# Optimization experiments

Hardware: AMD Instinct MI355X
Metric: run time of the kernel (lower is better)

## Reference

```python
import jax, jax.numpy as jnp
import numpy as np

N_NODES = 100000
NEG_SLOPE = 0.2

def _glorot(key, shape):
    lim = float(np.sqrt(6.0 / (shape[0] + shape[-1])))
    return jax.random.uniform(key, shape, jnp.float32, -lim, lim)

def setup_inputs() -> dict:
    key = jax.random.key(0)
    ks = jax.random.split(key, 12)
    x = jax.random.normal(ks[0], (N_NODES, 128), jnp.float32)
    edge_index = jax.random.randint(ks[1], (2, 3200000), 0, N_NODES).astype(jnp.int64)
    # layer 1: in=128, heads=2, out=8
    W1 = _glorot(ks[2], (128, 16)); a_src1 = _glorot(ks[3], (2, 8)); a_dst1 = _glorot(ks[4], (2, 8)); b1 = jnp.zeros((16,), jnp.float32)
    # layer 2: in=16, heads=2, out=4
    W2 = _glorot(ks[5], (16, 8)); a_src2 = _glorot(ks[6], (2, 4)); a_dst2 = _glorot(ks[7], (2, 4)); b2 = jnp.zeros((8,), jnp.float32)
    # layer 3: in=8, heads=1, out=4
    W3 = _glorot(ks[8], (8, 4)); a_src3 = _glorot(ks[9], (1, 4)); a_dst3 = _glorot(ks[10], (1, 4)); b3 = jnp.zeros((4,), jnp.float32)
    Wc = _glorot(ks[11], (4, 2)); bc = jnp.zeros((2,), jnp.float32)
    return {"x": x, "edge_index": edge_index,
            "W1": W1, "a_src1": a_src1, "a_dst1": a_dst1, "b1": b1,
            "W2": W2, "a_src2": a_src2, "a_dst2": a_dst2, "b2": b2,
            "W3": W3, "a_src3": a_src3, "a_dst3": a_dst3, "b3": b3,
            "Wc": Wc, "bc": bc}

def gat_layer(x, src, dst, W, a_src, a_dst, b, H, C):
    # PyG GATConv: linear -> per-node attention terms -> per-edge leaky_relu -> segment softmax over dst -> scatter-sum
    N = x.shape[0]
    h = (x @ W).reshape(N, H, C)                         # [N,H,C]
    alpha_s = jnp.sum(h * a_src, axis=-1)                # [N,H]
    alpha_d = jnp.sum(h * a_dst, axis=-1)                # [N,H]
    e = jax.nn.leaky_relu(alpha_s[src] + alpha_d[dst], NEG_SLOPE)  # [E,H]
    m = jax.ops.segment_max(e, dst, num_segments=N)      # [N,H]
    ex = jnp.exp(e - m[dst])
    denom = jax.ops.segment_sum(ex, dst, num_segments=N)
    alpha = ex / (denom[dst] + 1e-16)                    # [E,H]
    out = jax.ops.segment_sum(h[src] * alpha[:, :, None], dst, num_segments=N)  # [N,H,C]
    return out.reshape(N, H * C) + b

def reference(x, edge_index, W1, a_src1, a_dst1, b1, W2, a_src2, a_dst2, b2, W3, a_src3, a_dst3, b3, Wc, bc):
    N = x.shape[0]
    loop = jnp.arange(N, dtype=edge_index.dtype)
    src = jnp.concatenate([edge_index[0], loop])  # add_self_loops=True (PyG default)
    dst = jnp.concatenate([edge_index[1], loop])
    h = jax.nn.relu(gat_layer(x, src, dst, W1, a_src1, a_dst1, b1, 2, 8))
    h = jax.nn.relu(gat_layer(h, src, dst, W2, a_src2, a_dst2, b2, 2, 4))
    # dropout p=0.5 is identity in eval mode
    h = gat_layer(h, src, dst, W3, a_src3, a_dst3, b3, 1, 4)
    return h @ Wc + bc
```

## Files before the change

kernel.cpp:

```cpp
#include <hip/hip_runtime.h>

#define TB 256
#define NGRP 8
#define NB_P 512
#define TBP 256
#define NBKT 256
#define SORT_T 1024
#define STG_CAP 14336
#define STG2_CAP 6656

typedef int      i4v __attribute__((ext_vector_type(4)));
typedef float    f4v __attribute__((ext_vector_type(4)));
typedef _Float16 h4v __attribute__((ext_vector_type(4)));
typedef _Float16 h8v __attribute__((ext_vector_type(8)));

struct __align__(16) Rec2 { _Float16 h[8]; float as[2]; float pad[2]; };
struct __align__(16) Rec3 { _Float16 h[4]; float as; float pad; };

static __device__ __forceinline__ float leaky(float x) {
  return x > 0.f ? x : 0.2f * x;
}


__global__ void __launch_bounds__(TB)
k_scatter_node1(const int* __restrict__ srcA, const int* __restrict__ dstA,
                int* __restrict__ cnt, int* __restrict__ loffG,
                int* __restrict__ epkPriv, int E4, int E, unsigned M, int R,
                int CH4, int CHP,
                const float* __restrict__ xin, const float* __restrict__ W1,
                const float* __restrict__ a_src, const float* __restrict__ a_dst,
                _Float16* __restrict__ hout, float* __restrict__ as_,
                float* __restrict__ ad_, int N) {
  __shared__ __align__(16) char smem[33552];
  const int t = threadIdx.x;
  if (blockIdx.x < NB_P) {
    const int kblk = blockIdx.x;
    int* lc   = (int*)smem;
    int* loff = (int*)(smem + 4096);
    int* lcur = (int*)(smem + 5136);
    int* stg  = (int*)(smem + 6160);
    for (int i = t; i < 4 * NBKT; i += TBP) lc[i] = 0;
    __syncthreads();
    int* lcw = lc + (t >> 6) * NBKT;
    const int bstart = kblk * CH4;
    const int bend = min(E4, bstart + CH4);
    const i4v* d4 = reinterpret_cast<const i4v*>(dstA);
    const i4v* s4 = reinterpret_cast<const i4v*>(srcA);
    for (int i = bstart + t; i < bend; i += TBP) {
      i4v d = d4[i];
#pragma unroll
      for (int k = 0; k < 4; ++k) atomicAdd(&lcw[__umulhi((unsigned)d[k], M)], 1);
    }
    if (kblk == NB_P - 1) {
      for (int i = E4 * 4 + t; i < E; i += TBP)
        atomicAdd(&lcw[__umulhi((unsigned)dstA[i], M)], 1);
    }
    __syncthreads();
    int c = 0;
    if (t < NBKT) {
      c = lc[t] + lc[NBKT + t] + lc[2 * NBKT + t] + lc[3 * NBKT + t];
      loff[t] = c;
    }
    __syncthreads();
    for (int o = 1; o < NBKT; o <<= 1) {
      int u = (t < NBKT && t >= o) ? loff[t - o] : 0;
      __syncthreads();
      if (t < NBKT) loff[t] += u;
      __syncthreads();
    }
    if (t < NBKT) {
      int excl = loff[t] - c;
      cnt[t * NB_P + kblk] = c;
      loffG[kblk * NBKT + t] = excl;
      lcur[t] = excl;
      loff[t] = excl;
      if (t == NBKT - 1) loff[NBKT] = excl + c;
    }
    __syncthreads();
    for (int i = bstart + t; i < bend; i += TBP) {
      i4v d = d4[i];
      i4v sv = __builtin_nontemporal_load(&s4[i]);
#pragma unroll
      for (int k = 0; k < 4; ++k) {
        int dd = d[k];
        int b = __umulhi((unsigned)dd, M);
        int pos = atomicAdd(&lcur[b], 1);
        stg[pos] = ((dd - b * R) << 17) | sv[k];
      }
    }
    if (kblk == NB_P - 1) {
      for (int i = E4 * 4 + t; i < E; i += TBP) {
        int dd = dstA[i];
        int b = __umulhi((unsigned)dd, M);
        int pos = atomicAdd(&lcur[b], 1);
        stg[pos] = ((dd - b * R) << 17) | srcA[i];
      }
    }
    __syncthreads();
    const int total = loff[NBKT];
    int* dst = epkPriv + (size_t)kblk * CHP;
    for (int i = t; i < total; i += TBP) dst[i] = stg[i];
  } else {
    constexpr int IN = 128, OUT = 16, SPLIT = 4, NPB = TB / SPLIT, PIN4 = IN / SPLIT / 4;
    float* Ws = (float*)smem;
    float* As = (float*)(smem + 8192);
    float* Ad = (float*)(smem + 8256);
    const int bid = blockIdx.x - NB_P;
    for (int i = t; i < IN * OUT; i += TB) Ws[i] = W1[i];
    if (t < OUT) {
      As[t] = a_src[t];
      Ad[t] = a_dst[t];
    }
    __syncthreads();
    const int j = t & (SPLIT - 1);
    const int n = bid * NPB + t / SPLIT;
    if (n >= N) return;
    float acc[OUT];
#pragma unroll
    for (int q = 0; q < OUT; ++q) acc[q] = 0.f;
    const f4v* x4 = reinterpret_cast<const f4v*>(xin + (size_t)n * IN + j * (IN / SPLIT));
#pragma unroll
    for (int k4 = 0; k4 < PIN4; ++k4) {
      f4v xv = __builtin_nontemporal_load(&x4[k4]);
      const int kb = j * (IN / SPLIT) + 4 * k4;
#pragma unroll
      for (int q = 0; q < OUT; ++q) {
        acc[q] += xv[0] * Ws[(kb + 0) * OUT + q];
        acc[q] += xv[1] * Ws[(kb + 1) * OUT + q];
        acc[q] += xv[2] * Ws[(kb + 2) * OUT + q];
        acc[q] += xv[3] * Ws[(kb + 3) * OUT + q];
      }
    }
#pragma unroll
    for (int o = 1; o < SPLIT; o <<= 1) {
#pragma unroll
      for (int q = 0; q < OUT; ++q) acc[q] += __shfl_xor(acc[q], o);
    }
    if (j < OUT / 4) {
      h4v v;
      v[0] = (_Float16)acc[4 * j + 0];
      v[1] = (_Float16)acc[4 * j + 1];
      v[2] = (_Float16)acc[4 * j + 2];
      v[3] = (_Float16)acc[4 * j + 3];
      reinterpret_cast<h4v*>(hout + (size_t)n * OUT)[j] = v;
    }
    if (j < 2) {
      float ss = 0.f, dd = 0.f;
#pragma unroll
      for (int c = 0; c < 8; ++c) {
        ss += acc[j * 8 + c] * As[j * 8 + c];
        dd += acc[j * 8 + c] * Ad[j * 8 + c];
      }
      as_[n * 2 + j] = ss;
      ad_[n * 2 + j] = dd;
    }
  }
}

__global__ void k_bscan1(const int* __restrict__ cnt, int* __restrict__ off,
                         int* __restrict__ colTotal) {
  __shared__ int sh[NB_P];
  const int t = threadIdx.x;
  const int b = blockIdx.x;
  int v = cnt[b * NB_P + t];
  sh[t] = v;
  __syncthreads();
  for (int o = 1; o < NB_P; o <<= 1) {
    int u = (t >= o) ? sh[t - o] : 0;
    __syncthreads();
    sh[t] += u;
    __syncthreads();
  }
  off[b * NB_P + t] = sh[t] - v;
  if (t == NB_P - 1) colTotal[b] = sh[t];
}

__global__ void k_bscan2(const int* __restrict__ colTotal, int* __restrict__ bucketBase) {
  __shared__ int sh[NBKT];
  const int t = threadIdx.x;
  int v = colTotal[t];
  sh[t] = v;
  __syncthreads();
  for (int o = 1; o < NBKT; o <<= 1) {
    int u = (t >= o) ? sh[t - o] : 0;
    __syncthreads();
    sh[t] += u;
    __syncthreads();
  }
  bucketBase[t] = sh[t] - v;
  if (t == NBKT - 1) bucketBase[NBKT] = sh[t];
}

__global__ void k_bsort(const int* __restrict__ epkPriv, const int* __restrict__ off,
                        const int* __restrict__ loffG, const int* __restrict__ bucketBase,
                        int* __restrict__ rowStart, int* __restrict__ colIdx,
                        int N, int R, int E, int CHP) {
  __shared__ int offRow[NB_P];
  __shared__ int loffCol[NB_P];
  __shared__ int sc[512];
  __shared__ int stg[STG_CAP];
  const int b = (blockIdx.x & (NGRP - 1)) * (NBKT / NGRP) + (blockIdx.x >> 3);
  const int lo = bucketBase[b], hi = bucketBase[b + 1];
  const int cntB = hi - lo;
  const int nodeLo = b * R;
  const int nN = min(R, N - nodeLo);
  const int t = threadIdx.x;
  if (t < NB_P) {
    offRow[t] = off[b * NB_P + t];
    loffCol[t] = loffG[t * NBKT + b];
  }
  if (t < 512) sc[t] = 0;
  __syncthreads();
  auto fetch = [&](int i) -> int {
    int loQ = 0, hiQ = NB_P;
#pragma unroll
    for (int it = 0; it < 9; ++it) {
      int mid = (loQ + hiQ) >> 1;
      if (offRow[mid] <= i) loQ = mid; else hiQ = mid;
    }
    return epkPriv[(size_t)loQ * CHP + loffCol[loQ] + (i - offRow[loQ])];
  };
  for (int i = t; i < cntB; i += SORT_T) {
    int pk = fetch(i);
    atomicAdd(&sc[pk >> 17], 1);
  }
  __syncthreads();
  int own = (t < 512) ? sc[t] : 0;
  for (int o = 1; o < 512; o <<= 1) {
    int u = (t < 512 && t >= o) ? sc[t - o] : 0;
    __syncthreads();
    if (t < 512) sc[t] += u;
    __syncthreads();
  }
  if (t < nN) rowStart[nodeLo + t] = lo + sc[t] - own;
  if (b == NBKT - 1 && t == 0) rowStart[N] = E;
  if (t < 512) sc[t] -= own;
  __syncthreads();
  for (int i = t; i < cntB; i += SORT_T) {
    int pk = fetch(i);
    int pos = atomicAdd(&sc[pk >> 17], 1);
    stg[pos] = pk & 0x1FFFF;
  }
  __syncthreads();
  for (int i = t; i < cntB; i += SORT_T) colIdx[lo + i] = stg[i];
}


__global__ void k_edge12(const int* __restrict__ rowStart, const int* __restrict__ colIdx,
                         const _Float16* __restrict__ h1, const float* __restrict__ as_,
                         const float* __restrict__ ad_, const float* __restrict__ b1,
                         const float* __restrict__ W2, const float* __restrict__ as2w,
                         const float* __restrict__ ad2w, Rec2* __restrict__ r2,
                         float* __restrict__ ad2, int N, int R8) {
  constexpr int L = 2, S = 4, LS = 8, NPB = TB / LS;
  __shared__ float Ws2[128], A2s[8], A2d[8], B1s[16];
  if (threadIdx.x < 128) Ws2[threadIdx.x] = W2[threadIdx.x];
  if (threadIdx.x < 8) {
    A2s[threadIdx.x] = as2w[threadIdx.x];
    A2d[threadIdx.x] = ad2w[threadIdx.x];
  }
  if (threadIdx.x < 16) B1s[threadIdx.x] = b1[threadIdx.x];
  __syncthreads();
  const int g = blockIdx.x & (NGRP - 1);
  const int lb = blockIdx.x / NGRP;
  const int lane = threadIdx.x % LS;
  const int sub = lane >> 1;
  const int j = lane & 1;
  const int n = g * R8 + lb * NPB + threadIdx.x / LS;
  const int nEnd = min((g + 1) * R8, N);
  if (n >= nEnd) return;
  const float adv = ad_[n * 2 + j];
  const int start = rowStart[n];
  const int end = rowStart[n + 1];
  float s = 0.f, acc[8];
#pragma unroll
  for (int q = 0; q < 8; ++q) acc[q] = 0.f;
  if (sub == 0) {
    float p = __expf(leaky(as_[n * 2 + j] + adv));
    h8v a0 = reinterpret_cast<const h8v*>(h1 + (size_t)n * 16)[j];
    s = p;
#pragma unroll
    for (int q = 0; q < 8; ++q) acc[q] = p * (float)a0[q];
  }
  const int base = start & ~3;
  const int nch = (end - base + 3) >> 2;
  i4v cv;
  if (sub < nch) cv = *reinterpret_cast<const i4v*>(colIdx + base + 4 * sub);
  for (int t = sub; t < nch; t += S) {
    i4v nxt = cv;
    if (t + S < nch) nxt = *reinterpret_cast<const i4v*>(colIdx + base + 4 * (t + S));
    const int i0 = base + 4 * t;
#pragma unroll
    for (int k = 0; k < 4; ++k) {
      const bool ok = (i0 + k >= start) && (i0 + k < end);
      const int src = ok ? cv[k] : n;
      h8v hv = reinterpret_cast<const h8v*>(h1 + (size_t)src * 16)[j];
      float e = as_[src * 2 + j];
      float p = ok ? __expf(leaky(e + adv)) : 0.f;
      s += p;
#pragma unroll
      for (int q = 0; q < 8; ++q) acc[q] += p * (float)hv[q];
    }
    cv = nxt;
  }
#pragma unroll
  for (int off = L; off < LS; off <<= 1) {
    s += __shfl_xor(s, off);
#pragma unroll
    for (int q = 0; q < 8; ++q) acc[q] += __shfl_xor(acc[q], off);
  }
  if (sub == 0) {
    float inv = 1.f / (s + 1e-16f);
    float o1v[8];
#pragma unroll
    for (int q = 0; q < 8; ++q) o1v[q] = fmaxf(acc[q] * inv + B1s[j * 8 + q], 0.f);
    float h2p[8];
#pragma unroll
    for (int q = 0; q < 8; ++q) {
      float tacc = 0.f;
#pragma unroll
      for (int c = 0; c < 8; ++c) tacc += o1v[c] * Ws2[(j * 8 + c) * 8 + q];
      h2p[q] = tacc;
    }
    float h2f[8];
#pragma unroll
    for (int q = 0; q < 8; ++q) h2f[q] = h2p[q] + __shfl_xor(h2p[q], 1);
    h4v v;
#pragma unroll
    for (int q = 0; q < 4; ++q) v[q] = (_Float16)h2f[j * 4 + q];
    reinterpret_cast<h4v*>(r2[n].h)[j] = v;
    float ss = 0.f, dd = 0.f;
#pragma unroll
    for (int c = 0; c < 4; ++c) {
      ss += h2f[j * 4 + c] * A2s[j * 4 + c];
      dd += h2f[j * 4 + c] * A2d[j * 4 + c];
    }
    r2[n].as[j] = ss;
    ad2[n * 2 + j] = dd;
  }
}


__global__ void k_edge23(const int* __restrict__ rowStart, const int* __restrict__ colIdx,
                         const Rec2* __restrict__ r2, const float* __restrict__ ad_,
                         const float* __restrict__ b2, const float* __restrict__ W3,
                         const float* __restrict__ as3w, const float* __restrict__ ad3w,
                         Rec3* __restrict__ r3, float* __restrict__ ad3, int N, int R8) {
  constexpr int L = 2, S = 4, LS = 8, NPB = TB / LS;
  __shared__ float Ws3[32], A3s[4], A3d[4], B2s[8];
  if (threadIdx.x < 32) Ws3[threadIdx.x] = W3[threadIdx.x];
  if (threadIdx.x < 4) {
    A3s[threadIdx.x] = as3w[threadIdx.x];
    A3d[threadIdx.x] = ad3w[threadIdx.x];
  }
  if (threadIdx.x < 8) B2s[threadIdx.x] = b2[threadIdx.x];
  __syncthreads();
  const int g = blockIdx.x & (NGRP - 1);
  const int lb = blockIdx.x / NGRP;
  const int lane = threadIdx.x % LS;
  const int sub = lane >> 1;
  const int j = lane & 1;
  const int n = g * R8 + lb * NPB + threadIdx.x / LS;
  const int nEnd = min((g + 1) * R8, N);
  if (n >= nEnd) return;
  const float adv = ad_[n * 2 + j];
  const int start = rowStart[n];
  const int end = rowStart[n + 1];
  float s = 0.f, acc[4];
#pragma unroll
  for (int q = 0; q < 4; ++q) acc[q] = 0.f;
  if (sub == 0) {
    float p = __expf(leaky(r2[n].as[j] + adv));
    h4v a0 = reinterpret_cast<const h4v*>(r2[n].h)[j];
    s = p;
#pragma unroll
    for (int q = 0; q < 4; ++q) acc[q] = p * (float)a0[q];
  }
  const int base = start & ~3;
  const int nch = (end - base + 3) >> 2;
  i4v cv;
  if (sub < nch) cv = *reinterpret_cast<const i4v*>(colIdx + base + 4 * sub);
  for (int t = sub; t < nch; t += S) {
    i4v nxt = cv;
    if (t + S < nch) nxt = *reinterpret_cast<const i4v*>(colIdx + base + 4 * (t + S));
    const int i0 = base + 4 * t;
#pragma unroll
    for (int k = 0; k < 4; ++k) {
      const bool ok = (i0 + k >= start) && (i0 + k < end);
      const int src = ok ? cv[k] : n;
      h4v hv = reinterpret_cast<const h4v*>(r2[src].h)[j];
      float e = r2[src].as[j];
      float p = ok ? __expf(leaky(e + adv)) : 0.f;
      s += p;
#pragma unroll
      for (int q = 0; q < 4; ++q) acc[q] += p * (float)hv[q];
    }
    cv = nxt;
  }
#pragma unroll
  for (int off = L; off < LS; off <<= 1) {
    s += __shfl_xor(s, off);
#pragma unroll
    for (int q = 0; q < 4; ++q) acc[q] += __shfl_xor(acc[q], off);
  }
  if (sub == 0) {
    float inv = 1.f / (s + 1e-16f);
    float o2v[4];
#pragma unroll
    for (int q = 0; q < 4; ++q) o2v[q] = fmaxf(acc[q] * inv + B2s[j * 4 + q], 0.f);
    float h3p[4];
#pragma unroll
    for (int q = 0; q < 4; ++q) {
      float tacc = 0.f;
#pragma unroll
      for (int c = 0; c < 4; ++c) tacc += o2v[c] * Ws3[(j * 4 + c) * 4 + q];
      h3p[q] = tacc;
    }
    float h3f[4];
#pragma unroll
    for (int q = 0; q < 4; ++q) h3f[q] = h3p[q] + __shfl_xor(h3p[q], 1);
    if (j == 0) {
      Rec3 rec;
#pragma unroll
      for (int q = 0; q < 4; ++q) rec.h[q] = (_Float16)h3f[q];
      float ss = 0.f, dd = 0.f;
#pragma unroll
      for (int c = 0; c < 4; ++c) {
        ss += h3f[c] * A3s[c];
        dd += h3f[c] * A3d[c];
      }
      rec.as = ss;
      rec.pad = 0.f;
      r3[n] = rec;
      ad3[n] = dd;
    }
  }
}


__global__ void k_edge3(const int* __restrict__ rowStart, const int* __restrict__ colIdx,
                        const Rec3* __restrict__ r3, const float* __restrict__ ad_,
                        const float* __restrict__ b3, const float* __restrict__ Wc,
                        const float* __restrict__ bc, float* __restrict__ out,
                        int N, int R8) {
  constexpr int S = 8;
  constexpr int NPB = TB / S;
  const int g = blockIdx.x & (NGRP - 1);
  const int lb = blockIdx.x / NGRP;
  const int sub = threadIdx.x % S;
  const int n = g * R8 + lb * NPB + threadIdx.x / S;
  const int nEnd = min((g + 1) * R8, N);
  if (n >= nEnd) return;
  const float adv = ad_[n];
  const int start = rowStart[n];
  const int end = rowStart[n + 1];
  float s = 0.f, acc0 = 0.f, acc1 = 0.f, acc2 = 0.f, acc3 = 0.f;
  if (sub == 0) {
    Rec3 rec = r3[n];
    float p = __expf(leaky(rec.as + adv));
    s = p;
    acc0 = p * (float)rec.h[0];
    acc1 = p * (float)rec.h[1];
    acc2 = p * (float)rec.h[2];
    acc3 = p * (float)rec.h[3];
  }
  const int base = start & ~3;
  const int nch = (end - base + 3) >> 2;
  i4v cv;
  if (sub < nch) cv = *reinterpret_cast<const i4v*>(colIdx + base + 4 * sub);
  for (int t = sub; t < nch; t += S) {
    i4v nxt = cv;
    if (t + S < nch) nxt = *reinterpret_cast<const i4v*>(colIdx + base + 4 * (t + S));
    const int i0 = base + 4 * t;
#pragma unroll
    for (int k = 0; k < 4; ++k) {
      const bool ok = (i0 + k >= start) && (i0 + k < end);
      const int src = ok ? cv[k] : n;
      Rec3 rec = r3[src];
      float p = ok ? __expf(leaky(rec.as + adv)) : 0.f;
      s += p;
      acc0 += p * (float)rec.h[0];
      acc1 += p * (float)rec.h[1];
      acc2 += p * (float)rec.h[2];
      acc3 += p * (float)rec.h[3];
    }
    cv = nxt;
  }
#pragma unroll
  for (int off = 1; off < S; off <<= 1) {
    s += __shfl_xor(s, off);
    acc0 += __shfl_xor(acc0, off);
    acc1 += __shfl_xor(acc1, off);
    acc2 += __shfl_xor(acc2, off);
    acc3 += __shfl_xor(acc3, off);
  }
  if (sub == 0) {
    float inv = 1.f / (s + 1e-16f);
    float o0 = acc0 * inv + b3[0];
    float o1 = acc1 * inv + b3[1];
    float o2 = acc2 * inv + b3[2];
    float o3 = acc3 * inv + b3[3];
    float2 r;
    r.x = o0 * Wc[0] + o1 * Wc[2] + o2 * Wc[4] + o3 * Wc[6] + bc[0];
    r.y = o0 * Wc[1] + o1 * Wc[3] + o2 * Wc[5] + o3 * Wc[7] + bc[1];
    reinterpret_cast<float2*>(out)[n] = r;
  }
}


extern "C" void kernel_launch(void* const* d_in, const int* in_sizes, int n_in,
                              void* d_out, int out_size, void* d_ws, size_t ws_size,
                              hipStream_t stream) {
  const float* x    = (const float*)d_in[0];
  const int*   ei   = (const int*)d_in[1];
  const float* W1   = (const float*)d_in[2];
  const float* as1w = (const float*)d_in[3];
  const float* ad1w = (const float*)d_in[4];
  const float* b1   = (const float*)d_in[5];
  const float* W2   = (const float*)d_in[6];
  const float* as2w = (const float*)d_in[7];
  const float* ad2w = (const float*)d_in[8];
  const float* b2   = (const float*)d_in[9];
  const float* W3   = (const float*)d_in[10];
  const float* as3w = (const float*)d_in[11];
  const float* ad3w = (const float*)d_in[12];
  const float* b3   = (const float*)d_in[13];
  const float* Wc   = (const float*)d_in[14];
  const float* bc   = (const float*)d_in[15];
  float* out = (float*)d_out;

  const int N = in_sizes[0] / 128;
  const int E = in_sizes[1] / 2;
  const int* srcA = ei;
  const int* dstA = ei + E;

  char* p = (char*)d_ws;
  auto alloc = [&](size_t bytes) -> void* {
    void* r = (void*)p;
    p += (bytes + 255) & ~(size_t)255;
    return r;
  };
  const int E4  = E >> 2;
  const int CH4 = (E4 + NB_P - 1) / NB_P;
  const int CHP = CH4 * 4 + 8;

  int* cnt        = (int*)alloc((size_t)NBKT * NB_P * 4);
  int* off        = (int*)alloc((size_t)NBKT * NB_P * 4);
  int* loffG      = (int*)alloc((size_t)NB_P * NBKT * 4);
  int* colTotal   = (int*)alloc(NBKT * 4);
  int* bucketBase = (int*)alloc((NBKT + 1) * 4);
  int* rowStart   = (int*)alloc((size_t)(N + 1) * 4);
  int* epkPriv    = (int*)alloc((size_t)NB_P * CHP * 4);
  int* colIdx     = (int*)alloc((size_t)E * 4 + 256);
  _Float16* h1 = (_Float16*)alloc((size_t)N * 16 * 2);
  float* as1 = (float*)alloc((size_t)N * 2 * 4);
  float* ad1 = (float*)alloc((size_t)N * 2 * 4);
  Rec2* r2   = (Rec2*)alloc((size_t)N * sizeof(Rec2));
  float* ad2 = (float*)alloc((size_t)N * 2 * 4);
  Rec3* r3   = (Rec3*)alloc((size_t)N * sizeof(Rec3));
  float* ad3 = (float*)alloc((size_t)N * 4);

  const int R   = (N + NBKT - 1) / NBKT;
  const unsigned M = (unsigned)(((1ULL << 32) + R - 1) / R);
  const int R8  = R * (NBKT / NGRP);

  const int nb1 = (N + (TB / 4) - 1) / (TB / 4);
  const int ge8 = NGRP * ((R8 + (TB / 8) - 1) / (TB / 8));

  k_scatter_node1<<<NB_P + nb1, TB, 0, stream>>>(srcA, dstA, cnt, loffG, epkPriv,
                                                 E4, E, M, R, CH4, CHP,
                                                 x, W1, as1w, ad1w, h1, as1, ad1, N);
  k_bscan1<<<NBKT, NB_P, 0, stream>>>(cnt, off, colTotal);
  k_bscan2<<<1, NBKT, 0, stream>>>(colTotal, bucketBase);
  k_bsort<<<NBKT, SORT_T, 0, stream>>>(epkPriv, off, loffG, bucketBase, rowStart,
                                       colIdx, N, R, E, CHP);

  k_edge12<<<ge8, TB, 0, stream>>>(rowStart, colIdx, h1, as1, ad1, b1, W2, as2w, ad2w,
                                   r2, ad2, N, R8);
  k_edge23<<<ge8, TB, 0, stream>>>(rowStart, colIdx, r2, ad2, b2, W3, as3w, ad3w,
                                   r3, ad3, N, R8);
  k_edge3<<<ge8, TB, 0, stream>>>(rowStart, colIdx, r3, ad3, b3, Wc, bc, out, N, R8);
}
```

Before: 168.8 us.

## Double scatter blocks, cache edge loads in registers, recompute layer-1 source attention

Doubles the number of partition blocks in the bucket scatter and shrinks the per-block staging so more blocks fit per CU. The first pass now keeps up to four loaded dst/src vectors in registers so the second pass does not reload them from global memory. Layer-1 source attention is no longer stored per node; the edge kernel recomputes it from the fp16 features it already gathers, removing one random gather per edge. The bucket sort gains a direct-to-global fallback when a bucket overflows the shared staging buffer, and the scan kernel k_bscan1 is now launched with 1024 threads.

```diff
diff --git a/kernel.cpp b/kernel.cpp
--- a/kernel.cpp
+++ b/kernel.cpp
@@ -2,12 +2,13 @@
 
 #define TB 256
 #define NGRP 8
-#define NB_P 512
+#define NB_P 1024
 #define TBP 256
 #define NBKT 256
 #define SORT_T 1024
-#define STG_CAP 14336
-#define STG2_CAP 6656
+#define STG_CAP 13312
+#define STG2_CAP 3200
+#define RCAP 4
 
 typedef int      i4v __attribute__((ext_vector_type(4)));
 typedef float    f4v __attribute__((ext_vector_type(4)));
@@ -29,9 +30,8 @@
                 int CH4, int CHP,
                 const float* __restrict__ xin, const float* __restrict__ W1,
                 const float* __restrict__ a_src, const float* __restrict__ a_dst,
-                _Float16* __restrict__ hout, float* __restrict__ as_,
-                float* __restrict__ ad_, int N) {
-  __shared__ __align__(16) char smem[33552];
+                _Float16* __restrict__ hout, float* __restrict__ ad_, int N) {
+  __shared__ __align__(16) char smem[18960];
   const int t = threadIdx.x;
   if (blockIdx.x < NB_P) {
     const int kblk = blockIdx.x;
@@ -46,8 +46,12 @@
     const int bend = min(E4, bstart + CH4);
     const i4v* d4 = reinterpret_cast<const i4v*>(dstA);
     const i4v* s4 = reinterpret_cast<const i4v*>(srcA);
-    for (int i = bstart + t; i < bend; i += TBP) {
-      i4v d = d4[i];
+    i4v dr[RCAP], sr[RCAP];
+    int it1 = 0;
+    for (int i = bstart + t; i < bend; i += TBP, ++it1) {
+      i4v d = __builtin_nontemporal_load(&d4[i]);
+      i4v sv = __builtin_nontemporal_load(&s4[i]);
+      if (it1 < RCAP) { dr[it1] = d; sr[it1] = sv; }
 #pragma unroll
       for (int k = 0; k < 4; ++k) atomicAdd(&lcw[__umulhi((unsigned)d[k], M)], 1);
     }
@@ -77,9 +81,10 @@
       if (t == NBKT - 1) loff[NBKT] = excl + c;
     }
     __syncthreads();
-    for (int i = bstart + t; i < bend; i += TBP) {
-      i4v d = d4[i];
-      i4v sv = __builtin_nontemporal_load(&s4[i]);
+    int it2 = 0;
+    for (int i = bstart + t; i < bend; i += TBP, ++it2) {
+      i4v d = (it2 < RCAP) ? dr[it2] : d4[i];
+      i4v sv = (it2 < RCAP) ? sr[it2] : s4[i];
 #pragma unroll
       for (int k = 0; k < 4; ++k) {
         int dd = d[k];
@@ -103,14 +108,10 @@
   } else {
     constexpr int IN = 128, OUT = 16, SPLIT = 4, NPB = TB / SPLIT, PIN4 = IN / SPLIT / 4;
     float* Ws = (float*)smem;
-    float* As = (float*)(smem + 8192);
-    float* Ad = (float*)(smem + 8256);
+    float* Ad = (float*)(smem + 8192);
     const int bid = blockIdx.x - NB_P;
     for (int i = t; i < IN * OUT; i += TB) Ws[i] = W1[i];
-    if (t < OUT) {
-      As[t] = a_src[t];
-      Ad[t] = a_dst[t];
-    }
+    if (t < OUT) Ad[t] = a_dst[t];
     __syncthreads();
     const int j = t & (SPLIT - 1);
     const int n = bid * NPB + t / SPLIT;
@@ -145,13 +146,9 @@
       reinterpret_cast<h4v*>(hout + (size_t)n * OUT)[j] = v;
     }
     if (j < 2) {
-      float ss = 0.f, dd = 0.f;
-#pragma unroll
-      for (int c = 0; c < 8; ++c) {
-        ss += acc[j * 8 + c] * As[j * 8 + c];
-        dd += acc[j * 8 + c] * Ad[j * 8 + c];
-      }
-      as_[n * 2 + j] = ss;
+      float dd = 0.f;
+#pragma unroll
+      for (int c = 0; c < 8; ++c) dd += acc[j * 8 + c] * Ad[j * 8 + c];
       ad_[n * 2 + j] = dd;
     }
   }
@@ -205,16 +202,16 @@
   const int nodeLo = b * R;
   const int nN = min(R, N - nodeLo);
   const int t = threadIdx.x;
-  if (t < NB_P) {
-    offRow[t] = off[b * NB_P + t];
-    loffCol[t] = loffG[t * NBKT + b];
+  for (int i = t; i < NB_P; i += SORT_T) {
+    offRow[i] = off[b * NB_P + i];
+    loffCol[i] = loffG[i * NBKT + b];
   }
   if (t < 512) sc[t] = 0;
   __syncthreads();
   auto fetch = [&](int i) -> int {
     int loQ = 0, hiQ = NB_P;
 #pragma unroll
-    for (int it = 0; it < 9; ++it) {
+    for (int it = 0; it < 10; ++it) {
       int mid = (loQ + hiQ) >> 1;
       if (offRow[mid] <= i) loQ = mid; else hiQ = mid;
     }
@@ -236,30 +233,41 @@
   if (b == NBKT - 1 && t == 0) rowStart[N] = E;
   if (t < 512) sc[t] -= own;
   __syncthreads();
-  for (int i = t; i < cntB; i += SORT_T) {
-    int pk = fetch(i);
-    int pos = atomicAdd(&sc[pk >> 17], 1);
-    stg[pos] = pk & 0x1FFFF;
-  }
-  __syncthreads();
-  for (int i = t; i < cntB; i += SORT_T) colIdx[lo + i] = stg[i];
+  if (cntB <= STG_CAP) {
+    for (int i = t; i < cntB; i += SORT_T) {
+      int pk = fetch(i);
+      int pos = atomicAdd(&sc[pk >> 17], 1);
+      stg[pos] = pk & 0x1FFFF;
+    }
+    __syncthreads();
+    for (int i = t; i < cntB; i += SORT_T) colIdx[lo + i] = stg[i];
+  } else {
+    for (int i = t; i < cntB; i += SORT_T) {
+      int pk = fetch(i);
+      int pos = lo + atomicAdd(&sc[pk >> 17], 1);
+      colIdx[pos] = pk & 0x1FFFF;
+    }
+  }
 }
 
 
 __global__ void k_edge12(const int* __restrict__ rowStart, const int* __restrict__ colIdx,
-                         const _Float16* __restrict__ h1, const float* __restrict__ as_,
+                         const _Float16* __restrict__ h1, const float* __restrict__ as1w,
                          const float* __restrict__ ad_, const float* __restrict__ b1,
                          const float* __restrict__ W2, const float* __restrict__ as2w,
                          const float* __restrict__ ad2w, Rec2* __restrict__ r2,
                          float* __restrict__ ad2, int N, int R8) {
   constexpr int L = 2, S = 4, LS = 8, NPB = TB / LS;
-  __shared__ float Ws2[128], A2s[8], A2d[8], B1s[16];
+  __shared__ float Ws2[128], A1s[16], A2s[8], A2d[8], B1s[16];
   if (threadIdx.x < 128) Ws2[threadIdx.x] = W2[threadIdx.x];
+  if (threadIdx.x < 16) {
+    A1s[threadIdx.x] = as1w[threadIdx.x];
+    B1s[threadIdx.x] = b1[threadIdx.x];
+  }
   if (threadIdx.x < 8) {
     A2s[threadIdx.x] = as2w[threadIdx.x];
     A2d[threadIdx.x] = ad2w[threadIdx.x];
   }
-  if (threadIdx.x < 16) B1s[threadIdx.x] = b1[threadIdx.x];
   __syncthreads();
   const int g = blockIdx.x & (NGRP - 1);
   const int lb = blockIdx.x / NGRP;
@@ -270,14 +278,20 @@
   const int nEnd = min((g + 1) * R8, N);
   if (n >= nEnd) return;
   const float adv = ad_[n * 2 + j];
+  float aw[8];
+#pragma unroll
+  for (int c = 0; c < 8; ++c) aw[c] = A1s[j * 8 + c];
   const int start = rowStart[n];
   const int end = rowStart[n + 1];
   float s = 0.f, acc[8];
 #pragma unroll
   for (int q = 0; q < 8; ++q) acc[q] = 0.f;
   if (sub == 0) {
-    float p = __expf(leaky(as_[n * 2 + j] + adv));
     h8v a0 = reinterpret_cast<const h8v*>(h1 + (size_t)n * 16)[j];
+    float e = 0.f;
+#pragma unroll
+    for (int c = 0; c < 8; ++c) e += (float)a0[c] * aw[c];
+    float p = __expf(leaky(e + adv));
     s = p;
 #pragma unroll
     for (int q = 0; q < 8; ++q) acc[q] = p * (float)a0[q];
@@ -295,7 +309,9 @@
       const bool ok = (i0 + k >= start) && (i0 + k < end);
       const int src = ok ? cv[k] : n;
       h8v hv = reinterpret_cast<const h8v*>(h1 + (size_t)src * 16)[j];
-      float e = as_[src * 2 + j];
+      float e = 0.f;
+#pragma unroll
+      for (int c = 0; c < 8; ++c) e += (float)hv[c] * aw[c];
       float p = ok ? __expf(leaky(e + adv)) : 0.f;
       s += p;
 #pragma unroll
@@ -553,7 +569,6 @@
   int* epkPriv    = (int*)alloc((size_t)NB_P * CHP * 4);
   int* colIdx     = (int*)alloc((size_t)E * 4 + 256);
   _Float16* h1 = (_Float16*)alloc((size_t)N * 16 * 2);
-  float* as1 = (float*)alloc((size_t)N * 2 * 4);
   float* ad1 = (float*)alloc((size_t)N * 2 * 4);
   Rec2* r2   = (Rec2*)alloc((size_t)N * sizeof(Rec2));
   float* ad2 = (float*)alloc((size_t)N * 2 * 4);
@@ -569,13 +584,13 @@
 
   k_scatter_node1<<<NB_P + nb1, TB, 0, stream>>>(srcA, dstA, cnt, loffG, epkPriv,
                                                  E4, E, M, R, CH4, CHP,
-                                                 x, W1, as1w, ad1w, h1, as1, ad1, N);
+                                                 x, W1, as1w, ad1w, h1, ad1, N);
   k_bscan1<<<NBKT, NB_P, 0, stream>>>(cnt, off, colTotal);
   k_bscan2<<<1, NBKT, 0, stream>>>(colTotal, bucketBase);
   k_bsort<<<NBKT, SORT_T, 0, stream>>>(epkPriv, off, loffG, bucketBase, rowStart,
                                        colIdx, N, R, E, CHP);
 
-  k_edge12<<<ge8, TB, 0, stream>>>(rowStart, colIdx, h1, as1, ad1, b1, W2, as2w, ad2w,
+  k_edge12<<<ge8, TB, 0, stream>>>(rowStart, colIdx, h1, as1w, ad1, b1, W2, as2w, ad2w,
                                    r2, ad2, N, R8);
   k_edge23<<<ge8, TB, 0, stream>>>(rowStart, colIdx, r2, ad2, b2, W3, as3w, ad3w,
                                    r3, ad3, N, R8);
```

After: 160.9 us. 1.05x faster.
